# Kernel tuning notes

Measured on AMD Instinct MI355X. Metric: run time of the kernel, lower is better.

The kernel has to match this reference:

```python
import jax, jax.numpy as jnp
import numpy as np

B, T, F_IN = 64, 512, 264        # batch, time, total features
NONLSTM = 8                      # trailing non-LSTM feature channels
F_LSTM = F_IN - NONLSTM          # 256 features fed to the LSTM stack
HIDDEN = [512, 512]              # stacked OptimizedLSTMCell dims
DENSE = [512, 256]
PRED, FPP = 16, 4                # predictions, features_per_prediction


def _glorot(key, shape):
    fan_in, fan_out = shape[0], shape[1]
    lim = jnp.sqrt(6.0 / (fan_in + fan_out))
    return jax.random.uniform(key, shape, jnp.float32, -lim, lim)


def setup_inputs() -> dict:
    key = jax.random.key(0)
    ks = jax.random.split(key, 16)
    inp = {"x": jax.random.normal(ks[0], (B, T, F_IN), jnp.float32)}
    # LSTM layer params: Wi [in,4H] (no bias on input proj), Wh [H,4H], b [4H]
    in_dim = F_LSTM
    for j, h in enumerate(HIDDEN):
        inp[f"Wi{j}"] = _glorot(ks[1 + 3 * j], (in_dim, 4 * h))
        inp[f"Wh{j}"] = _glorot(ks[2 + 3 * j], (h, 4 * h))
        inp[f"b{j}"] = jnp.zeros((4 * h,), jnp.float32)
        in_dim = h
    # Dense head
    d_in = HIDDEN[-1] + NONLSTM
    for i, d in enumerate(DENSE):
        inp[f"Wd{i}"] = _glorot(ks[8 + 2 * i], (d_in, d))
        inp[f"bd{i}"] = jnp.zeros((d,), jnp.float32)
        d_in = d
    inp["Wf"] = _glorot(ks[14], (d_in, PRED * FPP))
    inp["bf"] = jnp.zeros((PRED * FPP,), jnp.float32)
    return inp


def lstm_layer(x, Wi, Wh, b):
    """flax OptimizedLSTMCell scanned over time. x: [B, T, F] -> [B, T, H]."""
    Bq = x.shape[0]
    H = Wh.shape[0]
    xw = jnp.einsum('btf,fg->btg', x, Wi)  # precompute input projections

    def step(carry, z_in):
        c, h = carry
        z = z_in + h @ Wh + b
        i, f, g, o = jnp.split(z, 4, axis=-1)
        c = jax.nn.sigmoid(f) * c + jax.nn.sigmoid(i) * jnp.tanh(g)
        h = jax.nn.sigmoid(o) * jnp.tanh(c)
        return (c, h), h

    c0 = jnp.zeros((Bq, H), x.dtype)
    h0 = jnp.zeros((Bq, H), x.dtype)
    _, hs = jax.lax.scan(step, (c0, h0), jnp.swapaxes(xw, 0, 1))
    return jnp.swapaxes(hs, 0, 1)


def reference(x, Wi0, Wh0, b0, Wi1, Wh1, b1, Wd0, bd0, Wd1, bd1, Wf, bf):
    last_features = x[:, -1, -NONLSTM:]          # [B, 8]
    h = x[:, :, :-NONLSTM]                       # [B, T, 256]
    # single LSTM branch: history == T, downsample == 1
    h = lstm_layer(h, Wi0, Wh0, b0)
    h = lstm_layer(h, Wi1, Wh1, b1)
    out = h[:, -1, :]                            # [B, H]
    out = jnp.concatenate([out, last_features], axis=1)
    out = jax.nn.relu(out @ Wd0 + bd0)
    out = jax.nn.relu(out @ Wd1 + bd1)
    out = out @ Wf + bf
    out = out.reshape((-1, PRED, FPP))
    return jax.nn.sigmoid(out)
```

## Files before the change

kernel.cpp:

```cpp
#include <hip/hip_runtime.h>
#include <hip/hip_bf16.h>

typedef __hip_bfloat16 bf16;
typedef short bf16x8 __attribute__((ext_vector_type(8)));
typedef float f32x4 __attribute__((ext_vector_type(4)));
typedef unsigned long long u64;
typedef unsigned int u32;

#define MFMA16(A, B, C) __builtin_amdgcn_mfma_f32_16x16x32_bf16(A, B, C, 0, 0, 0)

__device__ __forceinline__ float sigf(float x) { return 1.f / (1.f + __expf(-x)); }
__device__ __forceinline__ float tanh_fast(float x) { return 2.f / (1.f + __expf(-2.f * x)) - 1.f; }

__device__ __forceinline__ bf16x8 ld16(const u64* p) {
  u64 lo = __hip_atomic_load(p, __ATOMIC_RELAXED, __HIP_MEMORY_SCOPE_SYSTEM);
  u64 hi = __hip_atomic_load(p + 1, __ATOMIC_RELAXED, __HIP_MEMORY_SCOPE_SYSTEM);
  union { u64 q[2]; bf16x8 v; } u;
  u.q[0] = lo; u.q[1] = hi;
  return u.v;
}

__device__ __forceinline__ bf16x8 pack8(float4 f0, float4 f1) {
  union { short s[8]; bf16x8 v8; } o;
  o.s[0] = __builtin_bit_cast(short, __float2bfloat16(f0.x));
  o.s[1] = __builtin_bit_cast(short, __float2bfloat16(f0.y));
  o.s[2] = __builtin_bit_cast(short, __float2bfloat16(f0.z));
  o.s[3] = __builtin_bit_cast(short, __float2bfloat16(f0.w));
  o.s[4] = __builtin_bit_cast(short, __float2bfloat16(f1.x));
  o.s[5] = __builtin_bit_cast(short, __float2bfloat16(f1.y));
  o.s[6] = __builtin_bit_cast(short, __float2bfloat16(f1.z));
  o.s[7] = __builtin_bit_cast(short, __float2bfloat16(f1.w));
  return o.v8;
}

__global__ __launch_bounds__(256) void transpose_k(const float* __restrict__ W,
                                                   bf16* __restrict__ WT,
                                                   int K, int N) {
  __shared__ bf16 tile[32][33];
  const int n0 = blockIdx.x * 32, k0 = blockIdx.y * 32;
  const int c = threadIdx.x & 31, r0 = threadIdx.x >> 5;
  for (int i = 0; i < 4; ++i) {
    int r = r0 + 8 * i;
    tile[r][c] = __float2bfloat16(W[(long)(k0 + r) * N + (n0 + c)]);
  }
  __syncthreads();
  for (int i = 0; i < 4; ++i) {
    int r = r0 + 8 * i;
    WT[(long)(n0 + r) * K + (k0 + c)] = tile[c][r];
  }
}

__device__ __forceinline__ void gather16_issue(const u64* __restrict__ mat, int m,
                                               int q, bf16x8* out) {
#pragma unroll
  for (int i = 0; i < 16; ++i) {
    const int s = i * 4 + q;
    out[i] = ld16(mat + ((long)(s << 6) + m) * 2);
  }
}

__device__ __forceinline__ void validate16(const u64* __restrict__ mat, int m,
                                           int q, bf16x8* out) {
#pragma unroll
  for (int i = 0; i < 16; ++i) {
    const u64* p = mat + ((long)((i * 4 + q) << 6) + m) * 2;
    union { bf16x8 v; u64 w[2]; } u;
    u.v = out[i];
    while (u.w[0] == ~0ull || u.w[1] == ~0ull) {
      __builtin_amdgcn_s_sleep(1);
      u.w[0] = __hip_atomic_load(p, __ATOMIC_RELAXED, __HIP_MEMORY_SCOPE_SYSTEM);
      u.w[1] = __hip_atomic_load(p + 1, __ATOMIC_RELAXED, __HIP_MEMORY_SCOPE_SYSTEM);
    }
    out[i] = u.v;
  }
}

__global__ __launch_bounds__(256, 1) void lstm2_fused_k(
    const float* __restrict__ x,
    const bf16* __restrict__ WiT0, const bf16* __restrict__ WhT0,
    const float* __restrict__ bias0,
    const bf16* __restrict__ WiT1, const bf16* __restrict__ WhT1,
    const float* __restrict__ bias1,
    u64* __restrict__ h1D, u64* __restrict__ h2D)
{
  __shared__ short Wis[32 * 520];
  __shared__ short Whs[32 * 520];
  __shared__ float zs[32 * 66];
  __shared__ __align__(16) bf16 hstage[64 * 8];

  const int layer = blockIdx.x >> 6;
  const int w = blockIdx.x & 63;
  const int tid = threadIdx.x;
  const int lane = tid & 63;
  const int wv = tid >> 6;
  const int q = lane >> 4;
  const int r = lane & 15;

  const int K_in = layer ? 512 : 256;
  const bf16* WiT = layer ? WiT1 : WiT0;
  const bf16* WhT = layer ? WhT1 : WhT0;
  const float* bias = layer ? bias1 : bias0;
  u64* houtD = layer ? h2D : h1D;

  for (int idx = tid; idx < 32 * 64; idx += 256) {
    const int j = idx >> 6, kc = idx & 63;
    const int zc = (j >> 3) * 512 + w * 8 + (j & 7);
    *(bf16x8*)(Whs + j * 520 + kc * 8) = *(const bf16x8*)(WhT + (long)zc * 512 + kc * 8);
  }
  const int csh = layer ? 6 : 5;
  const int cmask = (1 << csh) - 1;
  for (int idx = tid; idx < (32 << csh); idx += 256) {
    const int j = idx >> csh, kc = idx & cmask;
    const int zc = (j >> 3) * 512 + w * 8 + (j & 7);
    *(bf16x8*)(Wis + j * 520 + kc * 8) = *(const bf16x8*)(WiT + (long)zc * K_in + kc * 8);
  }

  const int m = wv * 16 + r;
  const short* wi0p = Wis + r * 520;
  const short* wi1p = Wis + (16 + r) * 520;
  const short* wh0p = Whs + r * 520;
  const short* wh1p = Whs + (16 + r) * 520;

  const int gb = tid & 63;
  const int gc0 = tid >> 6;
  float bias_r[2][4];
  for (int s = 0; s < 2; ++s)
    for (int g = 0; g < 4; ++g)
      bias_r[s][g] = bias[g * 512 + w * 8 + gc0 + 4 * s];
  float creg[2] = {0.f, 0.f};

  __syncthreads();

#pragma unroll 1
  for (int t = 0; t < 512; ++t) {
    f32x4 acc0 = {0.f, 0.f, 0.f, 0.f};
    f32x4 acc1 = {0.f, 0.f, 0.f, 0.f};

    if (layer == 0) {
      const float* row = x + ((long)m * 512 + t) * 264;
      float4 xf0[8], xf1[8];
#pragma unroll
      for (int i = 0; i < 8; ++i) {
        xf0[i] = *(const float4*)(row + i * 32 + q * 8);
        xf1[i] = *(const float4*)(row + i * 32 + q * 8 + 4);
      }
      bf16x8 ah[16];
      if (t > 0) gather16_issue(h1D + (long)(t - 1) * 8192, m, q, ah);
#pragma unroll
      for (int i = 0; i < 8; ++i) {
        const bf16x8 ax = pack8(xf0[i], xf1[i]);
        const int kk = i * 32;
        acc0 = MFMA16(ax, *(const bf16x8*)(wi0p + kk + q * 8), acc0);
        acc1 = MFMA16(ax, *(const bf16x8*)(wi1p + kk + q * 8), acc1);
      }
      if (t > 0) {
        validate16(h1D + (long)(t - 1) * 8192, m, q, ah);
#pragma unroll
        for (int i = 0; i < 16; ++i) {
          const int kk = i * 32;
          acc0 = MFMA16(ah[i], *(const bf16x8*)(wh0p + kk + q * 8), acc0);
          acc1 = MFMA16(ah[i], *(const bf16x8*)(wh1p + kk + q * 8), acc1);
        }
      }
    } else {
      bf16x8 ax[16], ah[16];
      gather16_issue(h1D + (long)t * 8192, m, q, ax);
      if (t > 0) gather16_issue(h2D + (long)(t - 1) * 8192, m, q, ah);
      validate16(h1D + (long)t * 8192, m, q, ax);
#pragma unroll
      for (int i = 0; i < 16; ++i) {
        const int kk = i * 32;
        acc0 = MFMA16(ax[i], *(const bf16x8*)(wi0p + kk + q * 8), acc0);
        acc1 = MFMA16(ax[i], *(const bf16x8*)(wi1p + kk + q * 8), acc1);
      }
      if (t > 0) {
        validate16(h2D + (long)(t - 1) * 8192, m, q, ah);
#pragma unroll
        for (int i = 0; i < 16; ++i) {
          const int kk = i * 32;
          acc0 = MFMA16(ah[i], *(const bf16x8*)(wh0p + kk + q * 8), acc0);
          acc1 = MFMA16(ah[i], *(const bf16x8*)(wh1p + kk + q * 8), acc1);
        }
      }
    }

    {
      const int brow = wv * 16 + q * 4;
      for (int i = 0; i < 4; ++i) zs[r * 66 + brow + i] = acc0[i];
      for (int i = 0; i < 4; ++i) zs[(16 + r) * 66 + brow + i] = acc1[i];
    }
    __syncthreads();

    for (int s = 0; s < 2; ++s) {
      const int c = gc0 + 4 * s;
      const float zi = zs[(c)*66 + gb] + bias_r[s][0];
      const float zf = zs[(8 + c) * 66 + gb] + bias_r[s][1];
      const float zg = zs[(16 + c) * 66 + gb] + bias_r[s][2];
      const float zo = zs[(24 + c) * 66 + gb] + bias_r[s][3];
      const float cnew = sigf(zf) * creg[s] + sigf(zi) * tanh_fast(zg);
      const float hnew = sigf(zo) * tanh_fast(cnew);
      creg[s] = cnew;
      hstage[gb * 8 + c] = __float2bfloat16(hnew);
    }
    __syncthreads();

    if (tid < 64) {
      const u64* src = (const u64*)(hstage + tid * 8);
      u64* dst = houtD + (((long)t * 64 + w) * 64 + tid) * 2;
      __hip_atomic_store(dst, src[0], __ATOMIC_RELAXED, __HIP_MEMORY_SCOPE_SYSTEM);
      __hip_atomic_store(dst + 1, src[1], __ATOMIC_RELAXED, __HIP_MEMORY_SCOPE_SYSTEM);
    }
  }
}

__global__ __launch_bounds__(256) void head_k(
    const u64* __restrict__ h2D,
    const float* __restrict__ x,
    const float* __restrict__ Wd0, const float* __restrict__ bd0,
    const float* __restrict__ Wd1, const float* __restrict__ bd1,
    const float* __restrict__ Wf, const float* __restrict__ bfv,
    float* __restrict__ out) {
  const int b = blockIdx.x, tid = threadIdx.x;
  __shared__ float in0[520];
  __shared__ float d0s[512];
  __shared__ float d1s[256];
  if (tid < 64) {
    const int s = tid;
    bf16x8 v = ld16(h2D + (((long)511 * 64 + s) * 64 + b) * 2);
    union { bf16x8 v8; short sh[8]; } u;
    u.v8 = v;
    for (int j = 0; j < 8; ++j)
      in0[s * 8 + j] = __bfloat162float(__builtin_bit_cast(bf16, u.sh[j]));
  }
  if (tid < 8) in0[512 + tid] = x[((long)(b * 512 + 511)) * 264 + 256 + tid];
  __syncthreads();
  for (int j = tid; j < 512; j += 256) {
    float a = bd0[j];
    for (int k = 0; k < 520; ++k) a += in0[k] * Wd0[(long)k * 512 + j];
    d0s[j] = fmaxf(a, 0.f);
  }
  __syncthreads();
  if (tid < 256) {
    const int j = tid;
    float a = bd1[j];
    for (int k = 0; k < 512; ++k) a += d0s[k] * Wd1[(long)k * 256 + j];
    d1s[j] = fmaxf(a, 0.f);
  }
  __syncthreads();
  if (tid < 64) {
    const int j = tid;
    float a = bfv[j];
    for (int k = 0; k < 256; ++k) a += d1s[k] * Wf[(long)k * 64 + j];
    out[b * 64 + j] = sigf(a);
  }
}

extern "C" void kernel_launch(void* const* d_in, const int* in_sizes, int n_in,
                              void* d_out, int out_size, void* d_ws, size_t ws_size,
                              hipStream_t stream) {
  const float* x   = (const float*)d_in[0];
  const float* Wi0 = (const float*)d_in[1];
  const float* Wh0 = (const float*)d_in[2];
  const float* b0  = (const float*)d_in[3];
  const float* Wi1 = (const float*)d_in[4];
  const float* Wh1 = (const float*)d_in[5];
  const float* b1  = (const float*)d_in[6];
  const float* Wd0 = (const float*)d_in[7];
  const float* bd0 = (const float*)d_in[8];
  const float* Wd1 = (const float*)d_in[9];
  const float* bd1 = (const float*)d_in[10];
  const float* Wf  = (const float*)d_in[11];
  const float* bf_ = (const float*)d_in[12];
  float* out = (float*)d_out;

  char* ws = (char*)d_ws;
  size_t off = 0;
  auto carve = [&](size_t bytes) {
    void* p = ws + off;
    off += (bytes + 255) & ~(size_t)255;
    return p;
  };
  bf16* WiT0 = (bf16*)carve((size_t)2048 * 256 * 2);
  bf16* WhT0 = (bf16*)carve((size_t)2048 * 512 * 2);
  bf16* WiT1 = (bf16*)carve((size_t)2048 * 512 * 2);
  bf16* WhT1 = (bf16*)carve((size_t)2048 * 512 * 2);
  u64*  h1D  = (u64*)carve((size_t)512 * 64 * 64 * 16);
  u64*  h2D  = (u64*)carve((size_t)512 * 64 * 64 * 16);

  hipMemsetAsync(h1D, 0xFF, (size_t)2 * 512 * 64 * 64 * 16, stream);

  transpose_k<<<dim3(2048 / 32, 256 / 32), 256, 0, stream>>>(Wi0, WiT0, 256, 2048);
  transpose_k<<<dim3(2048 / 32, 512 / 32), 256, 0, stream>>>(Wh0, WhT0, 512, 2048);
  transpose_k<<<dim3(2048 / 32, 512 / 32), 256, 0, stream>>>(Wi1, WiT1, 512, 2048);
  transpose_k<<<dim3(2048 / 32, 512 / 32), 256, 0, stream>>>(Wh1, WhT1, 512, 2048);

  lstm2_fused_k<<<128, 256, 0, stream>>>(x, WiT0, WhT0, b0, WiT1, WhT1, b1,
                                         h1D, h2D);

  head_k<<<64, 256, 0, stream>>>(h2D, x, Wd0, bd0, Wd1, bd1, Wf, bf_, out);
}
```

Baseline: 3.237 ms.

## Pin each LSTM layer to one XCD and keep recurrent state exchange XCD-local

Launches 256 blocks and has each read its hardware XCC_ID, then claims a slot with an atomic counter. Only 32 blocks on XCD 0 (layer 0) and 32 on XCD 1 (layer 1) stay, each owning 16 hidden columns. The recurrent h exchange inside a layer moves to a local buffer read with sc0 inline-asm loads, so it can be served from the shared L2 rather than system-scope atomics. The cross-layer h1 stream and the final h2 still go through system-scope stores. It also uses XOR-swizzled LDS weights, computes gates directly in registers (dropping the zs staging pass), and adds bounded spin guards. The risks are reliance on the scheduler spreading blocks across XCDs so each gets 32, halved block count per layer, and the guard timeout silently returning invalid data.

```diff
diff --git a/kernel.cpp b/kernel.cpp
--- a/kernel.cpp
+++ b/kernel.cpp
@@ -12,25 +12,91 @@
 __device__ __forceinline__ float sigf(float x) { return 1.f / (1.f + __expf(-x)); }
 __device__ __forceinline__ float tanh_fast(float x) { return 2.f / (1.f + __expf(-2.f * x)) - 1.f; }
 
-__device__ __forceinline__ bf16x8 ld16(const u64* p) {
-  u64 lo = __hip_atomic_load(p, __ATOMIC_RELAXED, __HIP_MEMORY_SCOPE_SYSTEM);
-  u64 hi = __hip_atomic_load(p + 1, __ATOMIC_RELAXED, __HIP_MEMORY_SCOPE_SYSTEM);
-  union { u64 q[2]; bf16x8 v; } u;
-  u.q[0] = lo; u.q[1] = hi;
-  return u.v;
-}
-
-__device__ __forceinline__ bf16x8 pack8(float4 f0, float4 f1) {
+__device__ __forceinline__ bf16x8 pack8(f32x4 f0, f32x4 f1) {
   union { short s[8]; bf16x8 v8; } o;
-  o.s[0] = __builtin_bit_cast(short, __float2bfloat16(f0.x));
-  o.s[1] = __builtin_bit_cast(short, __float2bfloat16(f0.y));
-  o.s[2] = __builtin_bit_cast(short, __float2bfloat16(f0.z));
-  o.s[3] = __builtin_bit_cast(short, __float2bfloat16(f0.w));
-  o.s[4] = __builtin_bit_cast(short, __float2bfloat16(f1.x));
-  o.s[5] = __builtin_bit_cast(short, __float2bfloat16(f1.y));
-  o.s[6] = __builtin_bit_cast(short, __float2bfloat16(f1.z));
-  o.s[7] = __builtin_bit_cast(short, __float2bfloat16(f1.w));
+  o.s[0] = __builtin_bit_cast(short, __float2bfloat16(f0[0]));
+  o.s[1] = __builtin_bit_cast(short, __float2bfloat16(f0[1]));
+  o.s[2] = __builtin_bit_cast(short, __float2bfloat16(f0[2]));
+  o.s[3] = __builtin_bit_cast(short, __float2bfloat16(f0[3]));
+  o.s[4] = __builtin_bit_cast(short, __float2bfloat16(f1[0]));
+  o.s[5] = __builtin_bit_cast(short, __float2bfloat16(f1[1]));
+  o.s[6] = __builtin_bit_cast(short, __float2bfloat16(f1[2]));
+  o.s[7] = __builtin_bit_cast(short, __float2bfloat16(f1[3]));
   return o.v8;
+}
+
+__device__ __forceinline__ void gl2_16(u64 base, f32x4 a[16]) {
+  asm volatile(
+      "global_load_dwordx4 %0, %16, off sc0\n\t"
+      "global_load_dwordx4 %1, %16, off offset:64 sc0\n\t"
+      "global_load_dwordx4 %2, %16, off offset:128 sc0\n\t"
+      "global_load_dwordx4 %3, %16, off offset:192 sc0\n\t"
+      "global_load_dwordx4 %4, %16, off offset:256 sc0\n\t"
+      "global_load_dwordx4 %5, %16, off offset:320 sc0\n\t"
+      "global_load_dwordx4 %6, %16, off offset:384 sc0\n\t"
+      "global_load_dwordx4 %7, %16, off offset:448 sc0\n\t"
+      "global_load_dwordx4 %8, %16, off offset:512 sc0\n\t"
+      "global_load_dwordx4 %9, %16, off offset:576 sc0\n\t"
+      "global_load_dwordx4 %10, %16, off offset:640 sc0\n\t"
+      "global_load_dwordx4 %11, %16, off offset:704 sc0\n\t"
+      "global_load_dwordx4 %12, %16, off offset:768 sc0\n\t"
+      "global_load_dwordx4 %13, %16, off offset:832 sc0\n\t"
+      "global_load_dwordx4 %14, %16, off offset:896 sc0\n\t"
+      "global_load_dwordx4 %15, %16, off offset:960 sc0\n\t"
+      "s_waitcnt vmcnt(0)"
+      : "=&v"(a[0]), "=&v"(a[1]), "=&v"(a[2]), "=&v"(a[3]),
+        "=&v"(a[4]), "=&v"(a[5]), "=&v"(a[6]), "=&v"(a[7]),
+        "=&v"(a[8]), "=&v"(a[9]), "=&v"(a[10]), "=&v"(a[11]),
+        "=&v"(a[12]), "=&v"(a[13]), "=&v"(a[14]), "=&v"(a[15])
+      : "v"(base)
+      : "memory");
+}
+
+__device__ __forceinline__ void gl2_valid(u64 base, f32x4 a[16]) {
+  gl2_16(base, a);
+  int guard = 0;
+  for (;;) {
+    u64 bad = 0;
+#pragma unroll
+    for (int i = 0; i < 16; ++i) {
+      union { f32x4 f; u64 w[2]; } u;
+      u.f = a[i];
+      bad |= (u.w[0] + 1 == 0) ? 1u : 0u;
+      bad |= (u.w[1] + 1 == 0) ? 1u : 0u;
+    }
+    if (!bad) return;
+    if (++guard > 20000) return;
+    __builtin_amdgcn_s_sleep(1);
+    gl2_16(base, a);
+  }
+}
+
+__device__ __forceinline__ void rem_issue(const u64* __restrict__ b, f32x4 a[16]) {
+#pragma unroll
+  for (int i = 0; i < 16; ++i) {
+    union { f32x4 f; u64 w[2]; } u;
+    u.w[0] = __hip_atomic_load(b + i * 8, __ATOMIC_RELAXED, __HIP_MEMORY_SCOPE_SYSTEM);
+    u.w[1] = __hip_atomic_load(b + i * 8 + 1, __ATOMIC_RELAXED, __HIP_MEMORY_SCOPE_SYSTEM);
+    a[i] = u.f;
+  }
+}
+
+__device__ __forceinline__ void rem_valid(const u64* __restrict__ b, f32x4 a[16]) {
+  int guard = 0;
+  for (;;) {
+    u64 bad = 0;
+#pragma unroll
+    for (int i = 0; i < 16; ++i) {
+      union { f32x4 f; u64 w[2]; } u;
+      u.f = a[i];
+      bad |= (u.w[0] + 1 == 0) ? 1u : 0u;
+      bad |= (u.w[1] + 1 == 0) ? 1u : 0u;
+    }
+    if (!bad) return;
+    if (++guard > 20000) return;
+    __builtin_amdgcn_s_sleep(1);
+    rem_issue(b, a);
+  }
 }
 
 __global__ __launch_bounds__(256) void transpose_k(const float* __restrict__ W,
@@ -50,171 +116,185 @@
   }
 }
 
-__device__ __forceinline__ void gather16_issue(const u64* __restrict__ mat, int m,
-                                               int q, bf16x8* out) {
-#pragma unroll
-  for (int i = 0; i < 16; ++i) {
-    const int s = i * 4 + q;
-    out[i] = ld16(mat + ((long)(s << 6) + m) * 2);
-  }
-}
-
-__device__ __forceinline__ void validate16(const u64* __restrict__ mat, int m,
-                                           int q, bf16x8* out) {
-#pragma unroll
-  for (int i = 0; i < 16; ++i) {
-    const u64* p = mat + ((long)((i * 4 + q) << 6) + m) * 2;
-    union { bf16x8 v; u64 w[2]; } u;
-    u.v = out[i];
-    while (u.w[0] == ~0ull || u.w[1] == ~0ull) {
-      __builtin_amdgcn_s_sleep(1);
-      u.w[0] = __hip_atomic_load(p, __ATOMIC_RELAXED, __HIP_MEMORY_SCOPE_SYSTEM);
-      u.w[1] = __hip_atomic_load(p + 1, __ATOMIC_RELAXED, __HIP_MEMORY_SCOPE_SYSTEM);
-    }
-    out[i] = u.v;
-  }
-}
-
 __global__ __launch_bounds__(256, 1) void lstm2_fused_k(
     const float* __restrict__ x,
     const bf16* __restrict__ WiT0, const bf16* __restrict__ WhT0,
     const float* __restrict__ bias0,
     const bf16* __restrict__ WiT1, const bf16* __restrict__ WhT1,
     const float* __restrict__ bias1,
-    u64* __restrict__ h1D, u64* __restrict__ h2D)
+    char* __restrict__ h1_loc, char* __restrict__ h2_loc,
+    u64* __restrict__ h1_rem,
+    u64* __restrict__ h2_rem,
+    u32* __restrict__ cnt)
 {
-  __shared__ short Wis[32 * 520];
-  __shared__ short Whs[32 * 520];
-  __shared__ float zs[32 * 66];
-  __shared__ __align__(16) bf16 hstage[64 * 8];
-
-  const int layer = blockIdx.x >> 6;
-  const int w = blockIdx.x & 63;
+  __shared__ short Wis[64 * 512];
+  __shared__ short Whs[64 * 512];
+  __shared__ __align__(16) short hstage[64 * 16];
+  __shared__ int role_sh[2];
+
   const int tid = threadIdx.x;
-  const int lane = tid & 63;
-  const int wv = tid >> 6;
-  const int q = lane >> 4;
-  const int r = lane & 15;
+  if (tid == 0) {
+    u32 xcd;
+    asm volatile("s_getreg_b32 %0, hwreg(HW_REG_XCC_ID)" : "=s"(xcd));
+    u32 slot = __hip_atomic_fetch_add(&cnt[xcd & 7], 1u, __ATOMIC_RELAXED,
+                                      __HIP_MEMORY_SCOPE_AGENT);
+    role_sh[0] = (int)(xcd & 7);
+    role_sh[1] = (int)slot;
+  }
+  __syncthreads();
+  const int xcd = role_sh[0];
+  const int slot = role_sh[1];
+  if (!((xcd == 0 || xcd == 1) && slot < 32)) return;
+  const int layer = xcd;
+  const int cg = slot;
+
+  const int lane = tid & 63, wv = tid >> 6, q = lane >> 4, r = lane & 15;
+  const int m = wv * 16 + r;
+  const int swz = r & 7;
 
   const int K_in = layer ? 512 : 256;
   const bf16* WiT = layer ? WiT1 : WiT0;
   const bf16* WhT = layer ? WhT1 : WhT0;
   const float* bias = layer ? bias1 : bias0;
-  u64* houtD = layer ? h2D : h1D;
-
-  for (int idx = tid; idx < 32 * 64; idx += 256) {
+  char* hloc = layer ? h2_loc : h1_loc;
+
+  for (int idx = tid; idx < 64 * 64; idx += 256) {
     const int j = idx >> 6, kc = idx & 63;
-    const int zc = (j >> 3) * 512 + w * 8 + (j & 7);
-    *(bf16x8*)(Whs + j * 520 + kc * 8) = *(const bf16x8*)(WhT + (long)zc * 512 + kc * 8);
-  }
-  const int csh = layer ? 6 : 5;
-  const int cmask = (1 << csh) - 1;
-  for (int idx = tid; idx < (32 << csh); idx += 256) {
-    const int j = idx >> csh, kc = idx & cmask;
-    const int zc = (j >> 3) * 512 + w * 8 + (j & 7);
-    *(bf16x8*)(Wis + j * 520 + kc * 8) = *(const bf16x8*)(WiT + (long)zc * K_in + kc * 8);
-  }
-
-  const int m = wv * 16 + r;
-  const short* wi0p = Wis + r * 520;
-  const short* wi1p = Wis + (16 + r) * 520;
-  const short* wh0p = Whs + r * 520;
-  const short* wh1p = Whs + (16 + r) * 520;
-
-  const int gb = tid & 63;
-  const int gc0 = tid >> 6;
-  float bias_r[2][4];
-  for (int s = 0; s < 2; ++s)
-    for (int g = 0; g < 4; ++g)
-      bias_r[s][g] = bias[g * 512 + w * 8 + gc0 + 4 * s];
-  float creg[2] = {0.f, 0.f};
+    const int zc = (j >> 4) * 512 + cg * 16 + (j & 15);
+    *(bf16x8*)((char*)Whs + j * 1024 + ((kc ^ (j & 7)) << 4)) =
+        *(const bf16x8*)(WhT + (long)zc * 512 + kc * 8);
+  }
+  const int csh = layer ? 6 : 5, cm = (1 << csh) - 1;
+  const int rowb = K_in * 2;
+  for (int idx = tid; idx < (64 << csh); idx += 256) {
+    const int j = idx >> csh, kc = idx & cm;
+    const int zc = (j >> 4) * 512 + cg * 16 + (j & 15);
+    *(bf16x8*)((char*)Wis + j * rowb + ((kc ^ (j & 7)) << 4)) =
+        *(const bf16x8*)(WiT + (long)zc * K_in + kc * 8);
+  }
+
+  float br[4];
+#pragma unroll
+  for (int g = 0; g < 4; ++g) br[g] = bias[g * 512 + cg * 16 + r];
+  float creg[4] = {0.f, 0.f, 0.f, 0.f};
+
+  const u64 gbase = (u64)hloc + (u64)m * 1024 + (u64)(q * 16);
 
   __syncthreads();
 
 #pragma unroll 1
   for (int t = 0; t < 512; ++t) {
-    f32x4 acc0 = {0.f, 0.f, 0.f, 0.f};
-    f32x4 acc1 = {0.f, 0.f, 0.f, 0.f};
+    f32x4 acc[4];
+#pragma unroll
+    for (int nf = 0; nf < 4; ++nf) {
+      acc[nf][0] = 0.f; acc[nf][1] = 0.f; acc[nf][2] = 0.f; acc[nf][3] = 0.f;
+    }
 
     if (layer == 0) {
-      const float* row = x + ((long)m * 512 + t) * 264;
-      float4 xf0[8], xf1[8];
-#pragma unroll
-      for (int i = 0; i < 8; ++i) {
-        xf0[i] = *(const float4*)(row + i * 32 + q * 8);
-        xf1[i] = *(const float4*)(row + i * 32 + q * 8 + 4);
-      }
-      bf16x8 ah[16];
-      if (t > 0) gather16_issue(h1D + (long)(t - 1) * 8192, m, q, ah);
-#pragma unroll
-      for (int i = 0; i < 8; ++i) {
-        const bf16x8 ax = pack8(xf0[i], xf1[i]);
-        const int kk = i * 32;
-        acc0 = MFMA16(ax, *(const bf16x8*)(wi0p + kk + q * 8), acc0);
-        acc1 = MFMA16(ax, *(const bf16x8*)(wi1p + kk + q * 8), acc1);
+      const float* xr = x + ((long)m * 512 + t) * 264;
+      f32x4 xf[8][2];
+#pragma unroll
+      for (int kt = 0; kt < 8; ++kt) {
+        xf[kt][0] = __builtin_nontemporal_load((const f32x4*)(xr + kt * 32 + q * 8));
+        xf[kt][1] = __builtin_nontemporal_load((const f32x4*)(xr + kt * 32 + q * 8 + 4));
+      }
+      f32x4 ah[16];
+      if (t > 0) gl2_valid(gbase + (u64)(t - 1) * 65536, ah);
+      bf16x8 ax[8];
+#pragma unroll
+      for (int kt = 0; kt < 8; ++kt) ax[kt] = pack8(xf[kt][0], xf[kt][1]);
+#pragma unroll
+      for (int nf = 0; nf < 4; ++nf) {
+        const char* wb = (const char*)Wis + (nf * 16 + r) * 512;
+#pragma unroll
+        for (int kt = 0; kt < 8; ++kt)
+          acc[nf] = MFMA16(ax[kt], *(const bf16x8*)(wb + (((kt * 4 + q) ^ swz) << 4)),
+                           acc[nf]);
       }
       if (t > 0) {
-        validate16(h1D + (long)(t - 1) * 8192, m, q, ah);
-#pragma unroll
-        for (int i = 0; i < 16; ++i) {
-          const int kk = i * 32;
-          acc0 = MFMA16(ah[i], *(const bf16x8*)(wh0p + kk + q * 8), acc0);
-          acc1 = MFMA16(ah[i], *(const bf16x8*)(wh1p + kk + q * 8), acc1);
+#pragma unroll
+        for (int nf = 0; nf < 4; ++nf) {
+          const char* wb = (const char*)Whs + (nf * 16 + r) * 1024;
+#pragma unroll
+          for (int kt = 0; kt < 16; ++kt)
+            acc[nf] = MFMA16(__builtin_bit_cast(bf16x8, ah[kt]),
+                             *(const bf16x8*)(wb + (((kt * 4 + q) ^ swz) << 4)),
+                             acc[nf]);
         }
       }
     } else {
-      bf16x8 ax[16], ah[16];
-      gather16_issue(h1D + (long)t * 8192, m, q, ax);
-      if (t > 0) gather16_issue(h2D + (long)(t - 1) * 8192, m, q, ah);
-      validate16(h1D + (long)t * 8192, m, q, ax);
-#pragma unroll
-      for (int i = 0; i < 16; ++i) {
-        const int kk = i * 32;
-        acc0 = MFMA16(ax[i], *(const bf16x8*)(wi0p + kk + q * 8), acc0);
-        acc1 = MFMA16(ax[i], *(const bf16x8*)(wi1p + kk + q * 8), acc1);
-      }
+      f32x4 ax[16], ah[16];
+      const u64* remb = h1_rem + (u64)t * 8192 + (u64)(m * 128 + q * 2);
+      rem_issue(remb, ax);
       if (t > 0) {
-        validate16(h2D + (long)(t - 1) * 8192, m, q, ah);
-#pragma unroll
-        for (int i = 0; i < 16; ++i) {
-          const int kk = i * 32;
-          acc0 = MFMA16(ah[i], *(const bf16x8*)(wh0p + kk + q * 8), acc0);
-          acc1 = MFMA16(ah[i], *(const bf16x8*)(wh1p + kk + q * 8), acc1);
+        gl2_valid(gbase + (u64)(t - 1) * 65536, ah);
+#pragma unroll
+        for (int nf = 0; nf < 4; ++nf) {
+          const char* wb = (const char*)Whs + (nf * 16 + r) * 1024;
+#pragma unroll
+          for (int kt = 0; kt < 16; ++kt)
+            acc[nf] = MFMA16(__builtin_bit_cast(bf16x8, ah[kt]),
+                             *(const bf16x8*)(wb + (((kt * 4 + q) ^ swz) << 4)),
+                             acc[nf]);
         }
       }
-    }
-
-    {
-      const int brow = wv * 16 + q * 4;
-      for (int i = 0; i < 4; ++i) zs[r * 66 + brow + i] = acc0[i];
-      for (int i = 0; i < 4; ++i) zs[(16 + r) * 66 + brow + i] = acc1[i];
+      rem_valid(remb, ax);
+#pragma unroll
+      for (int nf = 0; nf < 4; ++nf) {
+        const char* wb = (const char*)Wis + (nf * 16 + r) * 1024;
+#pragma unroll
+        for (int kt = 0; kt < 16; ++kt)
+          acc[nf] = MFMA16(__builtin_bit_cast(bf16x8, ax[kt]),
+                           *(const bf16x8*)(wb + (((kt * 4 + q) ^ swz) << 4)),
+                           acc[nf]);
+      }
+    }
+
+#pragma unroll
+    for (int i = 0; i < 4; ++i) {
+      const float zi = acc[0][i] + br[0];
+      const float zf = acc[1][i] + br[1];
+      const float zg = acc[2][i] + br[2];
+      const float zo = acc[3][i] + br[3];
+      const float cnew = sigf(zf) * creg[i] + sigf(zi) * tanh_fast(zg);
+      const float hnew = sigf(zo) * tanh_fast(cnew);
+      creg[i] = cnew;
+      hstage[(wv * 16 + q * 4 + i) * 16 + r] =
+          __builtin_bit_cast(short, __float2bfloat16(hnew));
     }
     __syncthreads();
 
-    for (int s = 0; s < 2; ++s) {
-      const int c = gc0 + 4 * s;
-      const float zi = zs[(c)*66 + gb] + bias_r[s][0];
-      const float zf = zs[(8 + c) * 66 + gb] + bias_r[s][1];
-      const float zg = zs[(16 + c) * 66 + gb] + bias_r[s][2];
-      const float zo = zs[(24 + c) * 66 + gb] + bias_r[s][3];
-      const float cnew = sigf(zf) * creg[s] + sigf(zi) * tanh_fast(zg);
-      const float hnew = sigf(zo) * tanh_fast(cnew);
-      creg[s] = cnew;
-      hstage[gb * 8 + c] = __float2bfloat16(hnew);
+    if (tid < 64) {
+      const int row = tid;
+      const f32x4 v0 = *(const f32x4*)(hstage + row * 16);
+      const f32x4 v1 = *(const f32x4*)(hstage + row * 16 + 8);
+      const u64 dl = (u64)hloc + (u64)t * 65536 + (u64)(row * 1024 + cg * 32);
+      asm volatile(
+          "global_store_dwordx4 %0, %1, off sc0\n\t"
+          "global_store_dwordx4 %0, %2, off offset:16 sc0"
+          :: "v"(dl), "v"(v0), "v"(v1) : "memory");
+      union { f32x4 f[2]; u64 w[4]; } pu;
+      pu.f[0] = v0; pu.f[1] = v1;
+      if (layer == 0) {
+        u64* dr = h1_rem + (u64)t * 8192 + (u64)(row * 128 + cg * 4);
+        __hip_atomic_store(dr + 0, pu.w[0], __ATOMIC_RELAXED, __HIP_MEMORY_SCOPE_SYSTEM);
+        __hip_atomic_store(dr + 1, pu.w[1], __ATOMIC_RELAXED, __HIP_MEMORY_SCOPE_SYSTEM);
+        __hip_atomic_store(dr + 2, pu.w[2], __ATOMIC_RELAXED, __HIP_MEMORY_SCOPE_SYSTEM);
+        __hip_atomic_store(dr + 3, pu.w[3], __ATOMIC_RELAXED, __HIP_MEMORY_SCOPE_SYSTEM);
+      } else if (t == 511) {
+        u64* dr = h2_rem + (u64)(row * 128 + cg * 4);
+        __hip_atomic_store(dr + 0, pu.w[0], __ATOMIC_RELAXED, __HIP_MEMORY_SCOPE_SYSTEM);
+        __hip_atomic_store(dr + 1, pu.w[1], __ATOMIC_RELAXED, __HIP_MEMORY_SCOPE_SYSTEM);
+        __hip_atomic_store(dr + 2, pu.w[2], __ATOMIC_RELAXED, __HIP_MEMORY_SCOPE_SYSTEM);
+        __hip_atomic_store(dr + 3, pu.w[3], __ATOMIC_RELAXED, __HIP_MEMORY_SCOPE_SYSTEM);
+      }
     }
     __syncthreads();
-
-    if (tid < 64) {
-      const u64* src = (const u64*)(hstage + tid * 8);
-      u64* dst = houtD + (((long)t * 64 + w) * 64 + tid) * 2;
-      __hip_atomic_store(dst, src[0], __ATOMIC_RELAXED, __HIP_MEMORY_SCOPE_SYSTEM);
-      __hip_atomic_store(dst + 1, src[1], __ATOMIC_RELAXED, __HIP_MEMORY_SCOPE_SYSTEM);
-    }
   }
 }
 
 __global__ __launch_bounds__(256) void head_k(
-    const u64* __restrict__ h2D,
+    const u64* __restrict__ h2_rem,
     const float* __restrict__ x,
     const float* __restrict__ Wd0, const float* __restrict__ bd0,
     const float* __restrict__ Wd1, const float* __restrict__ bd1,
@@ -225,12 +305,15 @@
   __shared__ float d0s[512];
   __shared__ float d1s[256];
   if (tid < 64) {
-    const int s = tid;
-    bf16x8 v = ld16(h2D + (((long)511 * 64 + s) * 64 + b) * 2);
-    union { bf16x8 v8; short sh[8]; } u;
-    u.v8 = v;
+    const int c = tid;
+    u64 w0 = __hip_atomic_load(h2_rem + (long)b * 128 + c * 2, __ATOMIC_RELAXED,
+                               __HIP_MEMORY_SCOPE_SYSTEM);
+    u64 w1 = __hip_atomic_load(h2_rem + (long)b * 128 + c * 2 + 1, __ATOMIC_RELAXED,
+                               __HIP_MEMORY_SCOPE_SYSTEM);
+    union { u64 w[2]; short sh[8]; } u;
+    u.w[0] = w0; u.w[1] = w1;
     for (int j = 0; j < 8; ++j)
-      in0[s * 8 + j] = __bfloat162float(__builtin_bit_cast(bf16, u.sh[j]));
+      in0[c * 8 + j] = __bfloat162float(__builtin_bit_cast(bf16, u.sh[j]));
   }
   if (tid < 8) in0[512 + tid] = x[((long)(b * 512 + 511)) * 264 + 256 + tid];
   __syncthreads();
@@ -280,22 +363,29 @@
     off += (bytes + 255) & ~(size_t)255;
     return p;
   };
+  u32*  cnt  = (u32*)carve(256);
   bf16* WiT0 = (bf16*)carve((size_t)2048 * 256 * 2);
   bf16* WhT0 = (bf16*)carve((size_t)2048 * 512 * 2);
   bf16* WiT1 = (bf16*)carve((size_t)2048 * 512 * 2);
   bf16* WhT1 = (bf16*)carve((size_t)2048 * 512 * 2);
-  u64*  h1D  = (u64*)carve((size_t)512 * 64 * 64 * 16);
-  u64*  h2D  = (u64*)carve((size_t)512 * 64 * 64 * 16);
-
-  hipMemsetAsync(h1D, 0xFF, (size_t)2 * 512 * 64 * 64 * 16, stream);
+  char* h1_loc = (char*)carve((size_t)512 * 64 * 512 * 2);
+  char* h2_loc = (char*)carve((size_t)512 * 64 * 512 * 2);
+  u64*  h1_rem = (u64*)carve((size_t)512 * 64 * 512 * 2);
+  u64*  h2_rem = (u64*)carve((size_t)64 * 512 * 2);
+
+  (void)hipMemsetAsync(cnt, 0, 256, stream);
+  (void)hipMemsetAsync(h1_loc,
+                       0xFF,
+                       (size_t)3 * 512 * 64 * 512 * 2 + (size_t)64 * 512 * 2,
+                       stream);
 
   transpose_k<<<dim3(2048 / 32, 256 / 32), 256, 0, stream>>>(Wi0, WiT0, 256, 2048);
   transpose_k<<<dim3(2048 / 32, 512 / 32), 256, 0, stream>>>(Wh0, WhT0, 512, 2048);
   transpose_k<<<dim3(2048 / 32, 512 / 32), 256, 0, stream>>>(Wi1, WiT1, 512, 2048);
   transpose_k<<<dim3(2048 / 32, 512 / 32), 256, 0, stream>>>(Wh1, WhT1, 512, 2048);
 
-  lstm2_fused_k<<<128, 256, 0, stream>>>(x, WiT0, WhT0, b0, WiT1, WhT1, b1,
-                                         h1D, h2D);
-
-  head_k<<<64, 256, 0, stream>>>(h2D, x, Wd0, bd0, Wd1, bd1, Wf, bf_, out);
-}
+  lstm2_fused_k<<<256, 256, 0, stream>>>(x, WiT0, WhT0, b0, WiT1, WhT1, b1,
+                                         h1_loc, h2_loc, h1_rem, h2_rem, cnt);
+
+  head_k<<<64, 256, 0, stream>>>(h2_rem, x, Wd0, bd0, Wd1, bd1, Wf, bf_, out);
+}
```

After: 5.538 ms. +71.1%, slower.
